# Optimization experiments

Hardware: AMD Instinct MI355X
Metric: run time of the kernel (lower is better)

## Reference

```python
import jax, jax.numpy as jnp
import numpy as np

ALPHA = 0.4  # LeakyReLU negative slope used by the GAT


def _gat_head(h, W, a):
    # h: [N, F], W: [F, Fp], a: [2*Fp]; adjacency is all-ones so no masking
    Wh = h @ W                                   # [N, Fp]
    Fp = W.shape[1]
    e = jax.nn.leaky_relu(Wh @ a[:Fp][:, None] + (Wh @ a[Fp:])[None, :], ALPHA)
    att = jax.nn.softmax(e, axis=-1)             # [N, N]
    return att @ Wh                              # [N, Fp]


def _gat(h, W_heads, a_heads, W_gout, a_gout):
    # multi-head GAT: concat elu(head outputs), then single output attention layer
    heads = jax.vmap(_gat_head, in_axes=(None, 0, 0))(h, W_heads, a_heads)  # [H, N, Fp]
    x = jax.nn.elu(heads).transpose(1, 0, 2).reshape(h.shape[0], -1)        # [N, H*Fp]
    return jax.nn.elu(_gat_head(x, W_gout, a_gout))                          # [N, Cg]


def setup_inputs() -> dict:
    key = jax.random.key(0)
    ks = jax.random.split(key, 20)
    bs, R, S = 4, 512, 54
    h, w = 100, 152
    fc_dim, convs_dim4 = 1024, 512
    Cg, H, So = 256, 4, 128
    Fp = Cg // H
    sc = lambda k, shp, s=0.05: jax.random.normal(k, shp, dtype=jnp.float32) * s
    return {
        'region_f': jax.random.normal(ks[0], (bs * R, fc_dim), dtype=jnp.float32),
        'stuff_f': jax.random.normal(ks[1], (bs, convs_dim4, h, w), dtype=jnp.float32),
        'semseg_score': jax.random.normal(ks[2], (bs, S, h, w), dtype=jnp.float32),
        'W_rin': sc(ks[3], (fc_dim, Cg)), 'b_rin': jnp.zeros((Cg,), jnp.float32),
        'W_sin': sc(ks[4], (convs_dim4, Cg)), 'b_sin': jnp.zeros((Cg,), jnp.float32),
        'W_heads': sc(ks[5], (H, Cg, Fp), 0.1), 'a_heads': sc(ks[6], (H, 2 * Fp), 0.1),
        'W_gout': sc(ks[7], (H * Fp, Cg), 0.1), 'a_gout': sc(ks[8], (2 * Cg,), 0.1),
        'W_rout': sc(ks[9], (Cg, Cg)), 'b_rout': jnp.zeros((Cg,), jnp.float32),
        'W_sout': sc(ks[10], (Cg, So)), 'b_sout': jnp.zeros((So,), jnp.float32),
        'W_seg': sc(ks[11], (convs_dim4 + So, S)), 'b_seg': jnp.zeros((S,), jnp.float32),
    }


def reference(region_f, stuff_f, semseg_score,
              W_rin, b_rin, W_sin, b_sin,
              W_heads, a_heads, W_gout, a_gout,
              W_rout, b_rout, W_sout, b_sout,
              W_seg, b_seg):
    bs, Cd, h, w = stuff_f.shape
    S = semseg_score.shape[1]
    R = region_f.shape[0] // bs
    Cg = W_rin.shape[1]

    # node construction
    region_nodes = region_f @ W_rin + b_rin                           # [bs*R, Cg]
    score_flat = semseg_score.reshape(bs, S, h * w)
    class_center = jnp.einsum('bsn,bcn->bsc',
                              jax.nn.softmax(score_flat, axis=-1),
                              stuff_f.reshape(bs, Cd, h * w))          # [bs, S, Cd]
    class_nodes = class_center @ W_sin + b_sin                         # [bs, S, Cg]

    # per-image dense GAT over region + stuff nodes (batched via vmap)
    nodes = jnp.concatenate([region_nodes.reshape(bs, R, Cg), class_nodes], axis=1)
    graph_nodes = jax.vmap(lambda x: _gat(x, W_heads, a_heads, W_gout, a_gout))(nodes)
    new_region, new_class = graph_nodes[:, :R], graph_nodes[:, R:]

    # new box features: concat of original region features and projected graph features
    new_region_f = jnp.concatenate(
        [region_f, new_region.reshape(bs * R, Cg) @ W_rout + b_rout], axis=-1)

    # new stuff features: scatter class nodes back to pixels via class softmax
    new_class_nodes = new_class @ W_sout + b_sout                      # [bs, S, So]
    attn = jax.nn.softmax(score_flat, axis=1)                          # softmax over classes
    new_stuff = jnp.einsum('bsn,bso->bon', attn, new_class_nodes)      # [bs, So, h*w]
    new_stuff = new_stuff.reshape(bs, -1, h, w)

    # 1x1 conv seg head + x4 bilinear upsample (align_corners=False)
    seg_in = jnp.concatenate([stuff_f, new_stuff], axis=1)
    seg = jnp.einsum('bchw,co->bohw', seg_in, W_seg) + b_seg[None, :, None, None]
    segments = jax.image.resize(seg, (bs, S, 4 * h, 4 * w), method='bilinear')
    return new_region_f, segments
```

## Files before the change

### kernel.cpp

```cpp
#include <hip/hip_runtime.h>

#define HW 15200
#define SSD 54
#define NBATCH 4
#define NNODE 566
#define NPAD 576
#define CGD 256
#define CDD 512
#define NSPLIT 25
#define KSPAN 608

typedef __attribute__((ext_vector_type(4))) float f32x4;
typedef __attribute__((ext_vector_type(8))) short bf16x8;
typedef unsigned short ushort_t;

#define BT_RIN   0
#define BT_SIN   262144
#define BT_HEADS 393216
#define BT_GOUT  458752
#define BT_ROUT  524288
#define BT_SOUT  589824
#define BT_SEG2  622592
#define BT_TOTAL 630784

static constexpr long OFF_P     = 0;
static constexpr long OFF_CC    = OFF_P     + (long)NBATCH*SSD*HW;
static constexpr long OFF_NODES = OFF_CC    + (long)NBATCH*SSD*CDD;
static constexpr long OFF_WH    = OFF_NODES + (long)NBATCH*NNODE*CGD;
static constexpr long OFF_S1    = OFF_WH    + (long)16*NNODE*64;
static constexpr long OFF_S2    = OFF_S1    + 16*NPAD;
static constexpr long OFF_X     = OFF_S2    + 16*NPAD;
static constexpr long OFF_WH2   = OFF_X     + (long)NBATCH*NNODE*CGD;
static constexpr long OFF_S1B   = OFF_WH2   + (long)NBATCH*NNODE*CGD;
static constexpr long OFF_S2B   = OFF_S1B   + NBATCH*NPAD;
static constexpr long OFF_G     = OFF_S2B   + NBATCH*NPAD;
static constexpr long OFF_NCN   = OFF_G     + (long)NBATCH*NNODE*CGD;
static constexpr long OFF_SUMS  = OFF_NCN   + (long)NBATCH*SSD*128;
static constexpr long OFF_BT    = OFF_SUMS  + 256;
static constexpr long OFF_ASEG  = OFF_BT    + (BT_TOTAL/2 + 8);
static constexpr long OFF_SEG   = OFF_ASEG  + (long)NBATCH*64*576/2;
static constexpr long OFF_RFB   = OFF_SEG   + (long)NBATCH*SSD*HW;
static constexpr long OFF_WCOMB = OFF_RFB   + 1048576;
static constexpr long OFF_B2    = OFF_WCOMB + 8192;
static constexpr long OFF_ATTNB = OFF_B2    + 64;

__device__ inline float lrelu04(float x){ return x >= 0.f ? x : 0.4f*x; }
__device__ inline float eluf(float x){ return x > 0.f ? x : __expf(x) - 1.f; }
__device__ inline ushort_t f2bf(float f){
    unsigned u = __float_as_uint(f);
    return (ushort_t)((u + 0x7FFFu + ((u >> 16) & 1u)) >> 16);
}
__device__ inline float bf2f(ushort_t u){ return __uint_as_float((unsigned)u << 16); }
__device__ inline bf16x8 pack8(float4 lo, float4 hi){
    union { bf16x8 v; ushort_t u[8]; } p;
    p.u[0]=f2bf(lo.x); p.u[1]=f2bf(lo.y); p.u[2]=f2bf(lo.z); p.u[3]=f2bf(lo.w);
    p.u[4]=f2bf(hi.x); p.u[5]=f2bf(hi.y); p.u[6]=f2bf(hi.z); p.u[7]=f2bf(hi.w);
    return p.v;
}

__global__ __launch_bounds__(512)
void prep_softmax(const float* __restrict__ score, ushort_t* __restrict__ pb,
                  float* __restrict__ sums, ushort_t* __restrict__ attnb,
                  const float* __restrict__ rf, float* __restrict__ out_region,
                  ushort_t* __restrict__ rfb,
                  const float* __restrict__ W_seg, ushort_t* __restrict__ asegb,
                  const float* __restrict__ W_rin, const float* __restrict__ W_sin,
                  const float* __restrict__ W_heads, const float* __restrict__ W_gout,
                  const float* __restrict__ W_rout, const float* __restrict__ W_sout,
                  const float* __restrict__ b_sout,
                  ushort_t* __restrict__ bt, ushort_t* __restrict__ wcomb,
                  float* __restrict__ bias2, float* __restrict__ s1s2b_zero)
{
    int blk = blockIdx.x;
    int t = threadIdx.x;
    if (blk < 256) {
        int b = blk >> 6, s = blk & 63;
        ushort_t* prow = pb + ((long)b*64 + s)*HW;
        if (s >= SSD) {
            for (int i = t; i < HW; i += 512) prow[i] = 0;
            if (t == 0) sums[b*64 + s] = 1.f;
            return;
        }
        const float* row = score + ((long)b*SSD + s)*HW;
        __shared__ float red[8];
        float s_ = 0.f;
        for (int i = t; i < HW; i += 512) {
            float e = __expf(row[i]);
            s_ += e;
            prow[i] = f2bf(e);
        }
        #pragma unroll
        for (int off = 32; off >= 1; off >>= 1) s_ += __shfl_down(s_, off);
        if ((t & 63) == 0) red[t >> 6] = s_;
        __syncthreads();
        if (t == 0) {
            float tot = 0.f;
            #pragma unroll
            for (int u = 0; u < 8; ++u) tot += red[u];
            sums[b*64 + s] = tot;
        }
        return;
    }
    if (blk < 375) {
        long i = (long)(blk - 256)*512 + t;
        if (i >= (long)NBATCH*HW) return;
        int b = (int)(i / HW), n = (int)(i % HW);
        const float* sp = score + (long)b*SSD*HW + n;
        float v[SSD];
        float m = -1e30f;
        #pragma unroll
        for (int s = 0; s < SSD; ++s) { v[s] = sp[(long)s*HW]; m = fmaxf(m, v[s]); }
        float sum = 0.f;
        #pragma unroll
        for (int s = 0; s < SSD; ++s) { v[s] = __expf(v[s] - m); sum += v[s]; }
        float inv = 1.f / sum;
        ushort_t* ap = attnb + (long)b*64*HW + n;
        #pragma unroll
        for (int s = 0; s < SSD; ++s) ap[(long)s*HW] = f2bf(v[s] * inv);
        #pragma unroll
        for (int s = SSD; s < 64; ++s) ap[(long)s*HW] = 0;
        return;
    }
    long gid = (long)(blk - 375) * 512 + t;
    if (gid < 524288) {
        long row = gid / 256, col = gid % 256;
        float4 v = reinterpret_cast<const float4*>(rf)[gid];
        reinterpret_cast<float4*>(out_region)[row*320 + col] = v;
        union { ushort_t u[4]; uint2 q; } pk;
        pk.u[0]=f2bf(v.x); pk.u[1]=f2bf(v.y); pk.u[2]=f2bf(v.z); pk.u[3]=f2bf(v.w);
        reinterpret_cast<uint2*>(rfb)[gid] = pk.q;
        return;
    }
    gid -= 524288;
    if (gid < 131072) {
        int b = (int)(gid >> 15);
        int r = (int)(gid & 32767);
        int o = r >> 9, k = r & 511;
        asegb[(long)b*36864 + (long)o*576 + k] = f2bf(o < SSD ? W_seg[k*SSD + o] : 0.f);
        return;
    }
    gid -= 131072;
    if (gid < BT_TOTAL) {
        int i = (int)gid;
        float v;
        if (i < BT_SIN)        { int j=i;            int n=j>>10, k=j&1023; v = W_rin[k*256+n]; }
        else if (i < BT_HEADS) { int j=i-BT_SIN;     int n=j>>9,  k=j&511;  v = W_sin[k*256+n]; }
        else if (i < BT_GOUT)  { int j=i-BT_HEADS;   int h=j>>14, r=j&16383; int f=r>>8, k=r&255;
                                 v = W_heads[(h*256+k)*64+f]; }
        else if (i < BT_ROUT)  { int j=i-BT_GOUT;    int n=j>>8,  k=j&255;  v = W_gout[k*256+n]; }
        else if (i < BT_SOUT)  { int j=i-BT_ROUT;    int n=j>>8,  k=j&255;  v = W_rout[k*256+n]; }
        else if (i < BT_SEG2)  { int j=i-BT_SOUT;    int n=j>>8,  k=j&255;  v = W_sout[k*128+n]; }
        else                   { int j=i-BT_SEG2;    int o=j>>7,  k=j&127;
                                 v = (o < SSD) ? W_seg[(512+k)*SSD + o] : 0.f; }
        bt[i] = f2bf(v);
        return;
    }
    gid -= BT_TOTAL;
    if (gid < 16384) {
        int od = (int)(gid >> 8), k = (int)(gid & 255);
        float v = 0.f;
        if (od < SSD)
            for (int o = 0; o < 128; ++o)
                v += W_sout[k*128 + o] * W_seg[(512+o)*SSD + od];
        wcomb[(long)od*256 + k] = f2bf(v);
        return;
    }
    gid -= 16384;
    if (gid < 64) {
        int od = (int)gid;
        float v = 0.f;
        if (od < SSD)
            for (int o = 0; o < 128; ++o)
                v += b_sout[o] * W_seg[(512+o)*SSD + od];
        bias2[od] = v;
        return;
    }
    gid -= 64;
    if (gid < 2L*NBATCH*NPAD)
        s1s2b_zero[gid] = 0.f;
}

__global__ __launch_bounds__(256)
void cc_mfma_v3(const ushort_t* __restrict__ pb, const float* __restrict__ stuff,
                ushort_t* __restrict__ sbout, float* __restrict__ part)
{
    int bid = blockIdx.x;
    int g = (bid >> 6) * 8 + (bid & 7);
    if (g >= NSPLIT*NBATCH) return;
    int nt = (bid >> 3) & 7;
    int ks = g >> 2, b = g & 3;

    int w = threadIdx.x >> 6, l = threadIdx.x & 63;
    int lr = l & 15, lk = l >> 4;
    int n0 = nt*64 + w*16;
    const ushort_t* Prow = pb + ((long)b*64 + lr)*HW;
    const float*    Srow = stuff + ((long)b*CDD + n0 + lr)*HW;
    ushort_t*       Sout = sbout + ((long)b*CDD + n0 + lr)*HW;
    f32x4 acc[4] = {};
    int kbeg = ks * KSPAN;
    for (int k0 = kbeg; k0 < kbeg + KSPAN; k0 += 32) {
        int kk = k0 + lk*8;
        float4 lo = *(const float4*)&Srow[kk];
        float4 hi = *(const float4*)&Srow[kk + 4];
        bf16x8 bfv = pack8(lo, hi);
        *(bf16x8*)&Sout[kk] = bfv;
        #pragma unroll
        for (int mi = 0; mi < 4; ++mi) {
            bf16x8 af = *(const bf16x8*)&Prow[(long)mi*16*HW + kk];
            acc[mi] = __builtin_amdgcn_mfma_f32_16x16x32_bf16(af, bfv, acc[mi], 0, 0, 0);
        }
    }
    int c = n0 + lr;
    #pragma unroll
    for (int mi = 0; mi < 4; ++mi)
        #pragma unroll
        for (int r = 0; r < 4; ++r) {
            int m = mi*16 + lk*4 + r;
            part[(((long)b*NSPLIT + ks)*64 + m)*CDD + c] = acc[mi][r];
        }
}

__global__ __launch_bounds__(256)
void cc_reduce_kernel(const float* __restrict__ part, const float* __restrict__ sums,
                      float* __restrict__ cc)
{
    long i = (long)blockIdx.x * 256 + threadIdx.x;
    const long TOT = (long)NBATCH * SSD * CDD;
    if (i >= TOT) return;
    int b = (int)(i / (SSD * CDD));
    int rem = (int)(i % (SSD * CDD));
    int s = rem / CDD, c = rem % CDD;
    float acc = 0.f;
    for (int ks = 0; ks < NSPLIT; ++ks)
        acc += part[(((long)b*NSPLIT + ks)*64 + s)*CDD + c];
    cc[i] = acc * (1.f / sums[b*64 + s]);
}

template<bool AF32, int OUTMODE>
__device__ __forceinline__
void mm_body(int bx, int by, int bz,
             const void* __restrict__ Ap, const ushort_t* __restrict__ Bt,
             void* __restrict__ Cp, const float* __restrict__ bias,
             int M, int N, int K, int lda, int ldc,
             long sA, int zdivA, long sB, int zmodB, long sC)
{
    int z = bz;
    int w = threadIdx.x >> 6, l = threadIdx.x & 63;
    int lr = l & 15, lk = l >> 4;
    int m0 = bx * 64 + w * 16;
    int n0 = by * 64;
    const ushort_t* bt = Bt + (long)(z % zmodB) * sB;
    int mload = min(m0 + lr, M - 1);
    const float*    Af = (const float*)Ap    + (long)(z / zdivA) * sA + (long)mload * lda;
    const ushort_t* Ab = (const ushort_t*)Ap + (long)(z / zdivA) * sA + (long)mload * lda;
    f32x4 acc[4] = {};

    #pragma unroll 2
    for (int k0 = 0; k0 < K; k0 += 32) {
        int kk = k0 + lk * 8;
        bf16x8 af;
        if (AF32) {
            float4 lo = *(const float4*)&Af[kk];
            float4 hi = *(const float4*)&Af[kk + 4];
            af = pack8(lo, hi);
        } else {
            af = *(const bf16x8*)&Ab[kk];
        }
        #pragma unroll
        for (int j = 0; j < 4; ++j) {
            bf16x8 bf = *(const bf16x8*)&bt[(long)(n0 + j*16 + lr) * K + kk];
            acc[j] = __builtin_amdgcn_mfma_f32_16x16x32_bf16(af, bf, acc[j], 0, 0, 0);
        }
    }

    #pragma unroll
    for (int j = 0; j < 4; ++j) {
        int n = n0 + j*16 + lr;
        float bb = bias ? bias[n] : 0.f;
        #pragma unroll
        for (int r = 0; r < 4; ++r) {
            int m = m0 + lk*4 + r;
            if (OUTMODE == 2) {
                float v = acc[j][r] + bb;
                ((ushort_t*)Cp)[(long)z * sC + (long)n * ldc + m] =
                    (m < M) ? f2bf(v) : (ushort_t)0;
            } else {
                if (m >= M) continue;
                float v = acc[j][r] + bb;
                if (OUTMODE == 0)
                    ((float*)Cp)[(long)z * sC + (long)m * ldc + n] = v;
                else
                    ((ushort_t*)Cp)[(long)z * sC + (long)m * ldc + n] = f2bf(v);
            }
        }
    }
}

template<bool AF32, int OUTMODE>
__global__ __launch_bounds__(256)
void mm_mfma(const void* __restrict__ Ap, const ushort_t* __restrict__ Bt,
             void* __restrict__ Cp, const float* __restrict__ bias,
             int M, int N, int K, int lda, int ldc,
             long sA, int zdivA, long sB, int zmodB, long sC)
{
    mm_body<AF32, OUTMODE>(blockIdx.x, blockIdx.y, blockIdx.z,
                           Ap, Bt, Cp, bias, M, N, K, lda, ldc,
                           sA, zdivA, sB, zmodB, sC);
}

__global__ __launch_bounds__(256)
void nodes_both(const ushort_t* __restrict__ rfb, const ushort_t* __restrict__ btRin,
                const float* __restrict__ cc, const ushort_t* __restrict__ btSin,
                ushort_t* __restrict__ nodes,
                const float* __restrict__ b_rin, const float* __restrict__ b_sin)
{
    if (blockIdx.x < 8)
        mm_body<false, 1>(blockIdx.x, blockIdx.y, blockIdx.z,
                          rfb, btRin, nodes, b_rin,
                          512, 256, 1024, 1024, 256, 512L*1024, 1, 0, 1, (long)NNODE*CGD);
    else
        mm_body<true, 1>(0, blockIdx.y, blockIdx.z,
                         cc, btSin, nodes + 512L*CGD, b_sin,
                         SSD, 256, 512, 512, 256, (long)SSD*CDD, 1, 0, 1, (long)NNODE*CGD);
}

__global__ __launch_bounds__(256)
void rout_m2(const ushort_t* __restrict__ g_bf, const ushort_t* __restrict__ btRout,
             float* __restrict__ outreg, const float* __restrict__ b_rout,
             const ushort_t* __restrict__ wcomb, ushort_t* __restrict__ asegm2,
             const float* __restrict__ bias2)
{
    if (blockIdx.x < 8)
        mm_body<false, 0>(blockIdx.x, blockIdx.y, blockIdx.z,
                          g_bf, btRout, outreg, b_rout,
                          512, 256, 256, 256, 1280, (long)NNODE*CGD, 1, 0, 1, 512L*1280);
    else if (blockIdx.y == 0)
        mm_body<false, 2>(0, 0, blockIdx.z,
                          g_bf + 512L*CGD, wcomb, asegm2, bias2,
                          SSD, 64, 256, 256, 576, (long)NNODE*CGD, 1, 0, 1, 36864L);
}

__global__ __launch_bounds__(256)
void wht_heads(const ushort_t* __restrict__ nodes, const ushort_t* __restrict__ btHeads,
               ushort_t* __restrict__ wht, const float* __restrict__ a_heads,
               float* __restrict__ s1, float* __restrict__ s2)
{
    int bx = blockIdx.x, z = blockIdx.y;
    int w = threadIdx.x >> 6, l = threadIdx.x & 63;
    int lr = l & 15, lk = l >> 4;
    int m0 = bx*64 + w*16;
    const ushort_t* bt = btHeads + (long)(z & 3) * (64L*256);
    int mload = min(m0 + lr, NNODE - 1);
    const ushort_t* Ab = nodes + (long)(z >> 2)*((long)NNODE*CGD) + (long)mload*CGD;
    f32x4 acc[4] = {};

    #pragma unroll 2
    for (int k0 = 0; k0 < 256; k0 += 32) {
        int kk = k0 + lk*8;
        bf16x8 af = *(const bf16x8*)&Ab[kk];
        #pragma unroll
        for (int j = 0; j < 4; ++j) {
            bf16x8 bf = *(const bf16x8*)&bt[(long)(j*16 + lr)*256 + kk];
            acc[j] = __builtin_amdgcn_mfma_f32_16x16x32_bf16(af, bf, acc[j], 0, 0, 0);
        }
    }

    const float* av = a_heads + (long)(z & 3)*128;
    ushort_t* Wout = wht + (long)z*(64L*NPAD);
    float p1[4] = {0.f,0.f,0.f,0.f}, p2[4] = {0.f,0.f,0.f,0.f};
    #pragma unroll
    for (int j = 0; j < 4; ++j) {
        int f = j*16 + lr;
        float c1 = av[f], c2 = av[64 + f];
        #pragma unroll
        for (int r = 0; r < 4; ++r) {
            int m = m0 + lk*4 + r;
            float v = acc[j][r];
            Wout[(long)f*NPAD + m] = (m < NNODE) ? f2bf(v) : (ushort_t)0;
            if (m < NNODE) { p1[r] += v*c1; p2[r] += v*c2; }
        }
    }
    #pragma unroll
    for (int r = 0; r < 4; ++r)
        #pragma unroll
        for (int off = 1; off < 16; off <<= 1) {
            p1[r] += __shfl_xor(p1[r], off);
            p2[r] += __shfl_xor(p2[r], off);
        }
    if (lr == 0) {
        #pragma unroll
        for (int r = 0; r < 4; ++r) {
            int m = m0 + lk*4 + r;
            if (m < NNODE) {
                s1[(long)z*NPAD + m] = p1[r];
                s2[(long)z*NPAD + m] = p2[r];
            }
        }
    }
}

__global__ __launch_bounds__(256)
void wht2_gout(const ushort_t* __restrict__ xbuf, const ushort_t* __restrict__ btGout,
               ushort_t* __restrict__ wht2, const float* __restrict__ a_gout,
               float* __restrict__ s1b, float* __restrict__ s2b)
{
    int bx = blockIdx.x, by = blockIdx.y, z = blockIdx.z;
    int w = threadIdx.x >> 6, l = threadIdx.x & 63;
    int lr = l & 15, lk = l >> 4;
    int m0 = bx*64 + w*16;
    int n0 = by*64;
    int mload = min(m0 + lr, NNODE - 1);
    const ushort_t* Ab = xbuf + (long)z*((long)NNODE*CGD) + (long)mload*CGD;
    f32x4 acc[4] = {};

    #pragma unroll 2
    for (int k0 = 0; k0 < 256; k0 += 32) {
        int kk = k0 + lk*8;
        bf16x8 af = *(const bf16x8*)&Ab[kk];
        #pragma unroll
        for (int j = 0; j < 4; ++j) {
            bf16x8 bf = *(const bf16x8*)&btGout[(long)(n0 + j*16 + lr)*256 + kk];
            acc[j] = __builtin_amdgcn_mfma_f32_16x16x32_bf16(af, bf, acc[j], 0, 0, 0);
        }
    }

    ushort_t* Wout = wht2 + (long)z*(256L*NPAD);
    float p1[4] = {0.f,0.f,0.f,0.f}, p2[4] = {0.f,0.f,0.f,0.f};
    #pragma unroll
    for (int j = 0; j < 4; ++j) {
        int f = n0 + j*16 + lr;
        float c1 = a_gout[f], c2 = a_gout[256 + f];
        #pragma unroll
        for (int r = 0; r < 4; ++r) {
            int m = m0 + lk*4 + r;
            float v = acc[j][r];
            Wout[(long)f*NPAD + m] = (m < NNODE) ? f2bf(v) : (ushort_t)0;
            if (m < NNODE) { p1[r] += v*c1; p2[r] += v*c2; }
        }
    }
    #pragma unroll
    for (int r = 0; r < 4; ++r)
        #pragma unroll
        for (int off = 1; off < 16; off <<= 1) {
            p1[r] += __shfl_xor(p1[r], off);
            p2[r] += __shfl_xor(p2[r], off);
        }
    if (lr == 0) {
        #pragma unroll
        for (int r = 0; r < 4; ++r) {
            int m = m0 + lk*4 + r;
            if (m < NNODE) {
                atomicAdd(&s1b[(long)z*NPAD + m], p1[r]);
                atomicAdd(&s2b[(long)z*NPAD + m], p2[r]);
            }
        }
    }
}

template<int F, int HEADMODE>
__global__ __launch_bounds__(256)
void att_mfma(const ushort_t* __restrict__ WhTall, const float* __restrict__ s1v,
              const float* __restrict__ s2v, ushort_t* __restrict__ outbuf)
{
    constexpr int FT = F / 16;
    int z = blockIdx.y;
    const ushort_t* W  = WhTall + (long)z * F * NPAD;
    const float* s1 = s1v + (long)z * NPAD;
    const float* s2 = s2v + (long)z * NPAD;
    int w = threadIdx.x >> 6, l = threadIdx.x & 63;
    int lr = l & 15, lk = l >> 4;

    __shared__ float s2sh[NPAD];
    __shared__ float redm[4];
    float mxl = -1e30f;
    for (int i = threadIdx.x; i < NPAD; i += 256) {
        float v = (i < NNODE) ? s2[i] : -1e30f;
        s2sh[i] = v;
        mxl = fmaxf(mxl, v);
    }
    #pragma unroll
    for (int off = 32; off >= 1; off >>= 1) mxl = fmaxf(mxl, __shfl_down(mxl, off));
    if (l == 0) redm[w] = mxl;
    __syncthreads();
    float s2max = fmaxf(fmaxf(redm[0], redm[1]), fmaxf(redm[2], redm[3]));

    int m0 = blockIdx.x * 64 + w * 16;
    float s1r = s1[min(m0 + lr, NNODE - 1)];
    float mrow = lrelu04(s1r + s2max);

    union { bf16x8 v; ushort_t u[8]; } onesu;
    #pragma unroll
    for (int u = 0; u < 8; ++u) onesu.u[u] = 0x3F80;
    bf16x8 ones = onesu.v;

    f32x4 acc[FT] = {};
    f32x4 accw = {};

    for (int j0 = 0; j0 < NPAD; j0 += 32) {
        float wv[8];
        #pragma unroll
        for (int u = 0; u < 8; ++u) {
            float e = lrelu04(s1r + s2sh[j0 + lk*8 + u]);
            wv[u] = __expf(e - mrow);
        }
        float4 lo = {wv[0], wv[1], wv[2], wv[3]};
        float4 hi = {wv[4], wv[5], wv[6], wv[7]};
        bf16x8 af = pack8(lo, hi);
        accw = __builtin_amdgcn_mfma_f32_16x16x32_bf16(af, ones, accw, 0, 0, 0);
        #pragma unroll
        for (int ft = 0; ft < FT; ++ft) {
            bf16x8 bf = *(const bf16x8*)&W[(long)(ft*16 + lr)*NPAD + j0 + lk*8];
            acc[ft] = __builtin_amdgcn_mfma_f32_16x16x32_bf16(af, bf, acc[ft], 0, 0, 0);
        }
    }

    #pragma unroll
    for (int r = 0; r < 4; ++r) {
        int m = m0 + lk*4 + r;
        if (m >= NNODE) continue;
        float inv = 1.f / accw[r];
        #pragma unroll
        for (int ft = 0; ft < FT; ++ft) {
            int f = ft*16 + lr;
            float v = eluf(acc[ft][r] * inv);
            if (HEADMODE) {
                int b = z >> 2, h = z & 3;
                outbuf[((long)(b*NNODE + m))*CGD + h*64 + f] = f2bf(v);
            } else {
                outbuf[((long)(z*NNODE + m))*CGD + f] = f2bf(v);
            }
        }
    }
}

__global__ __launch_bounds__(256)
void seg_mfma(const ushort_t* __restrict__ stuffb, const ushort_t* __restrict__ attnb,
              const ushort_t* __restrict__ asegb, const float* __restrict__ b_seg,
              float* __restrict__ seg)
{
    int nt = blockIdx.x, b = blockIdx.y;
    int w = threadIdx.x >> 6, l = threadIdx.x & 63;
    int lr = l & 15, lk = l >> 4;
    int n0 = nt*128 + w*32;
    const ushort_t* A = asegb + (long)b*36864;
    const ushort_t* S = stuffb + (long)b*CDD*HW;
    const ushort_t* T = attnb + (long)b*64*HW;
    f32x4 acc[4][2] = {};
    int n1 = min(n0 + lr, HW-1);
    int n2 = min(n0 + 16 + lr, HW-1);

    for (int k0 = 0; k0 < 576; k0 += 32) {
        const ushort_t* Bsrc = (k0 < 512) ? S + (long)k0*HW : T + (long)(k0-512)*HW;
        long kb = (long)(lk*8)*HW;
        union { bf16x8 v; ushort_t u[8]; } b0, b1;
        #pragma unroll
        for (int u = 0; u < 8; ++u) {
            b0.u[u] = Bsrc[kb + (long)u*HW + n1];
            b1.u[u] = Bsrc[kb + (long)u*HW + n2];
        }
        #pragma unroll
        for (int ot = 0; ot < 4; ++ot) {
            bf16x8 af = *(const bf16x8*)&A[(ot*16 + lr)*576 + k0 + lk*8];
            acc[ot][0] = __builtin_amdgcn_mfma_f32_16x16x32_bf16(af, b0.v, acc[ot][0], 0,0,0);
            acc[ot][1] = __builtin_amdgcn_mfma_f32_16x16x32_bf16(af, b1.v, acc[ot][1], 0,0,0);
        }
    }

    #pragma unroll
    for (int ot = 0; ot < 4; ++ot) {
        #pragma unroll
        for (int r = 0; r < 4; ++r) {
            int o = ot*16 + lk*4 + r;
            if (o >= SSD) continue;
            float bb = b_seg[o];
            int na = n0 + lr, nb = n0 + 16 + lr;
            if (na < HW) seg[((long)b*SSD + o)*HW + na] = acc[ot][0][r] + bb;
            if (nb < HW) seg[((long)b*SSD + o)*HW + nb] = acc[ot][1][r] + bb;
        }
    }
}

__global__ __launch_bounds__(256)
void resize_v2_kernel(const float* __restrict__ seg, float* __restrict__ out)
{
    long u = (long)blockIdx.x * 256 + threadIdx.x;
    const long TOT4 = (long)NBATCH * SSD * 400 * 152;
    if (u >= TOT4) return;
    int m = (int)(u % 152);
    long r = u / 152;
    int y = (int)(r % 400);
    long c = r / 400;
    float fy = y * 0.25f - 0.375f;
    int y0 = (int)floorf(fy);
    float wy = fy - (float)y0;
    int y0c = max(y0, 0), y1c = min(y0 + 1, 99);
    const float* sp = seg + c * HW;
    int xm = max(m - 1, 0), xp = min(m + 1, 151);
    float r0a = sp[y0c * 152 + xm], r0b = sp[y0c * 152 + m], r0c = sp[y0c * 152 + xp];
    float r1a = sp[y1c * 152 + xm], r1b = sp[y1c * 152 + m], r1c = sp[y1c * 152 + xp];
    float ra = r0a + wy * (r1a - r0a);
    float rb = r0b + wy * (r1b - r0b);
    float rc = r0c + wy * (r1c - r0c);
    float4 o4;
    o4.x = 0.375f * ra + 0.625f * rb;
    o4.y = 0.125f * ra + 0.875f * rb;
    o4.z = 0.875f * rb + 0.125f * rc;
    o4.w = 0.625f * rb + 0.375f * rc;
    reinterpret_cast<float4*>(out)[u] = o4;
}

extern "C" void kernel_launch(void* const* d_in, const int* in_sizes, int n_in,
                              void* d_out, int out_size, void* d_ws, size_t ws_size,
                              hipStream_t stream)
{
    const float* region_f = (const float*)d_in[0];
    const float* stuff    = (const float*)d_in[1];
    const float* score    = (const float*)d_in[2];
    const float* W_rin    = (const float*)d_in[3];
    const float* b_rin    = (const float*)d_in[4];
    const float* W_sin    = (const float*)d_in[5];
    const float* b_sin    = (const float*)d_in[6];
    const float* W_heads  = (const float*)d_in[7];
    const float* a_heads  = (const float*)d_in[8];
    const float* W_gout   = (const float*)d_in[9];
    const float* a_gout   = (const float*)d_in[10];
    const float* W_rout   = (const float*)d_in[11];
    const float* b_rout   = (const float*)d_in[12];
    const float* W_sout   = (const float*)d_in[13];
    const float* b_sout   = (const float*)d_in[14];
    const float* W_seg    = (const float*)d_in[15];
    const float* b_seg    = (const float*)d_in[16];

    float* out = (float*)d_out;
    float* ws  = (float*)d_ws;

    ushort_t* pb   = (ushort_t*)(ws + OFF_P);
    float* cc      = ws + OFF_CC;
    ushort_t* nodes_bf = (ushort_t*)(ws + OFF_NODES);
    ushort_t* wht  = (ushort_t*)(ws + OFF_WH);
    float* s1      = ws + OFF_S1;
    float* s2      = ws + OFF_S2;
    ushort_t* xbuf_bf = (ushort_t*)(ws + OFF_X);
    ushort_t* wht2 = (ushort_t*)(ws + OFF_WH2);
    float* s1b     = ws + OFF_S1B;
    float* s2b     = ws + OFF_S2B;
    ushort_t* g_bf = (ushort_t*)(ws + OFF_G);
    float* sums    = ws + OFF_SUMS;
    ushort_t* bt   = (ushort_t*)(ws + OFF_BT);
    ushort_t* asegb = (ushort_t*)(ws + OFF_ASEG);
    float* segb    = ws + OFF_SEG;
    float* cc_p    = ws + OFF_SEG;
    ushort_t* rfb  = (ushort_t*)(ws + OFF_RFB);
    ushort_t* wcomb = (ushort_t*)(ws + OFF_WCOMB);
    float* bias2v  = ws + OFF_B2;
    ushort_t* attnb = (ushort_t*)(ws + OFF_ATTNB);

    float* out_region = out;
    float* out_seg    = out + 2048L*1280;
    ushort_t* stuffb  = (ushort_t*)out_seg;

    prep_softmax<<<2929, 512, 0, stream>>>(score, pb, sums, attnb,
                                           region_f, out_region, rfb, W_seg, asegb,
                                           W_rin, W_sin, W_heads, W_gout, W_rout, W_sout,
                                           b_sout, bt, wcomb, bias2v, s1b);

    cc_mfma_v3<<<832, 256, 0, stream>>>(pb, stuff, stuffb, cc_p);
    cc_reduce_kernel<<<(NBATCH*SSD*CDD + 255)/256, 256, 0, stream>>>(cc_p, sums, cc);

    nodes_both<<<dim3(9, 4, 4), 256, 0, stream>>>(
        rfb, bt + BT_RIN, cc, bt + BT_SIN, nodes_bf, b_rin, b_sin);

    wht_heads<<<dim3(9, 16), 256, 0, stream>>>(
        nodes_bf, bt + BT_HEADS, wht, a_heads, s1, s2);

    att_mfma<64, 1><<<dim3(9, 16), 256, 0, stream>>>(wht, s1, s2, xbuf_bf);

    wht2_gout<<<dim3(9, 4, 4), 256, 0, stream>>>(
        xbuf_bf, bt + BT_GOUT, wht2, a_gout, s1b, s2b);

    att_mfma<256, 0><<<dim3(9, NBATCH), 256, 0, stream>>>(wht2, s1b, s2b, g_bf);

    rout_m2<<<dim3(9, 4, 4), 256, 0, stream>>>(
        g_bf, bt + BT_ROUT, out_region + 1024, b_rout, wcomb, asegb + 512, bias2v);

    seg_mfma<<<dim3((HW+127)/128, NBATCH), 256, 0, stream>>>(
        stuffb, attnb, asegb, b_seg, segb);

    resize_v2_kernel<<<((long)NBATCH*SSD*400*152 + 255)/256, 256, 0, stream>>>(segb, out_seg);
}
```

Before: 321.9 us.

## Fuse GAT attention, gout projection, and rout/seg stages into fewer kernels

Merges the per-head attention with the output-layer weight projection into one kernel per batch, keeping head outputs in shared memory instead of a global buffer. Folds the class-node seg-weight projection into the output attention kernel, and merges the region output GEMM with the seg head GEMM into one launch. Replaces atomics with direct stores, which removes the zeroing pass. This cuts launches and global round-trips, but the fused graph kernels run on far fewer blocks with more serial work per block.

```diff
diff --git a/kernel.cpp b/kernel.cpp
--- a/kernel.cpp
+++ b/kernel.cpp
@@ -69,7 +69,7 @@
                   const float* __restrict__ W_rout, const float* __restrict__ W_sout,
                   const float* __restrict__ b_sout,
                   ushort_t* __restrict__ bt, ushort_t* __restrict__ wcomb,
-                  float* __restrict__ bias2, float* __restrict__ s1s2b_zero)
+                  float* __restrict__ bias2)
 {
     int blk = blockIdx.x;
     int t = threadIdx.x;
@@ -173,11 +173,7 @@
             for (int o = 0; o < 128; ++o)
                 v += b_sout[o] * W_seg[(512+o)*SSD + od];
         bias2[od] = v;
-        return;
-    }
-    gid -= 64;
-    if (gid < 2L*NBATCH*NPAD)
-        s1s2b_zero[gid] = 0.f;
+    }
 }
 
 __global__ __launch_bounds__(256)
@@ -296,18 +292,6 @@
     }
 }
 
-template<bool AF32, int OUTMODE>
-__global__ __launch_bounds__(256)
-void mm_mfma(const void* __restrict__ Ap, const ushort_t* __restrict__ Bt,
-             void* __restrict__ Cp, const float* __restrict__ bias,
-             int M, int N, int K, int lda, int ldc,
-             long sA, int zdivA, long sB, int zmodB, long sC)
-{
-    mm_body<AF32, OUTMODE>(blockIdx.x, blockIdx.y, blockIdx.z,
-                           Ap, Bt, Cp, bias, M, N, K, lda, ldc,
-                           sA, zdivA, sB, zmodB, sC);
-}
-
 __global__ __launch_bounds__(256)
 void nodes_both(const ushort_t* __restrict__ rfb, const ushort_t* __restrict__ btRin,
                 const float* __restrict__ cc, const ushort_t* __restrict__ btSin,
@@ -325,22 +309,6 @@
 }
 
 __global__ __launch_bounds__(256)
-void rout_m2(const ushort_t* __restrict__ g_bf, const ushort_t* __restrict__ btRout,
-             float* __restrict__ outreg, const float* __restrict__ b_rout,
-             const ushort_t* __restrict__ wcomb, ushort_t* __restrict__ asegm2,
-             const float* __restrict__ bias2)
-{
-    if (blockIdx.x < 8)
-        mm_body<false, 0>(blockIdx.x, blockIdx.y, blockIdx.z,
-                          g_bf, btRout, outreg, b_rout,
-                          512, 256, 256, 256, 1280, (long)NNODE*CGD, 1, 0, 1, 512L*1280);
-    else if (blockIdx.y == 0)
-        mm_body<false, 2>(0, 0, blockIdx.z,
-                          g_bf + 512L*CGD, wcomb, asegm2, bias2,
-                          SSD, 64, 256, 256, 576, (long)NNODE*CGD, 1, 0, 1, 36864L);
-}
-
-__global__ __launch_bounds__(256)
 void wht_heads(const ushort_t* __restrict__ nodes, const ushort_t* __restrict__ btHeads,
                ushort_t* __restrict__ wht, const float* __restrict__ a_heads,
                float* __restrict__ s1, float* __restrict__ s2)
@@ -400,42 +368,105 @@
 }
 
 __global__ __launch_bounds__(256)
-void wht2_gout(const ushort_t* __restrict__ xbuf, const ushort_t* __restrict__ btGout,
-               ushort_t* __restrict__ wht2, const float* __restrict__ a_gout,
-               float* __restrict__ s1b, float* __restrict__ s2b)
-{
-    int bx = blockIdx.x, by = blockIdx.y, z = blockIdx.z;
-    int w = threadIdx.x >> 6, l = threadIdx.x & 63;
+void att64_wht2(const ushort_t* __restrict__ whtAll, const float* __restrict__ s1v,
+                const float* __restrict__ s2v, const ushort_t* __restrict__ btGout,
+                ushort_t* __restrict__ wht2, const float* __restrict__ a_gout,
+                float* __restrict__ s1b, float* __restrict__ s2b)
+{
+    int bx = blockIdx.x, b = blockIdx.y;
+    int t = threadIdx.x;
+    int w = t >> 6, l = t & 63;
     int lr = l & 15, lk = l >> 4;
     int m0 = bx*64 + w*16;
-    int n0 = by*64;
-    int mload = min(m0 + lr, NNODE - 1);
-    const ushort_t* Ab = xbuf + (long)z*((long)NNODE*CGD) + (long)mload*CGD;
-    f32x4 acc[4] = {};
-
-    #pragma unroll 2
-    for (int k0 = 0; k0 < 256; k0 += 32) {
-        int kk = k0 + lk*8;
-        bf16x8 af = *(const bf16x8*)&Ab[kk];
-        #pragma unroll
-        for (int j = 0; j < 4; ++j) {
-            bf16x8 bf = *(const bf16x8*)&btGout[(long)(n0 + j*16 + lr)*256 + kk];
-            acc[j] = __builtin_amdgcn_mfma_f32_16x16x32_bf16(af, bf, acc[j], 0, 0, 0);
-        }
-    }
-
-    ushort_t* Wout = wht2 + (long)z*(256L*NPAD);
-    float p1[4] = {0.f,0.f,0.f,0.f}, p2[4] = {0.f,0.f,0.f,0.f};
-    #pragma unroll
-    for (int j = 0; j < 4; ++j) {
-        int f = n0 + j*16 + lr;
-        float c1 = a_gout[f], c2 = a_gout[256 + f];
+
+    __shared__ float s2sh[4][NPAD];
+    __shared__ float s2maxsh[4];
+    __shared__ ushort_t xst[64][264];
+
+    for (int i = t; i < 4*NPAD; i += 256) {
+        int h = i / NPAD, j = i % NPAD;
+        s2sh[h][j] = (j < NNODE) ? s2v[((long)(b*4 + h))*NPAD + j] : -1e30f;
+    }
+    if (bx == 8)
+        for (int i = t; i < 10*264; i += 256) xst[54 + i/264][i%264] = 0;
+    __syncthreads();
+    {
+        float mx = -1e30f;
+        for (int q = 0; q < 9; ++q) mx = fmaxf(mx, s2sh[w][l + 64*q]);
+        #pragma unroll
+        for (int off = 32; off >= 1; off >>= 1) mx = fmaxf(mx, __shfl_down(mx, off));
+        if (l == 0) s2maxsh[w] = mx;
+    }
+    __syncthreads();
+
+    union { bf16x8 v; ushort_t u[8]; } onesu;
+    #pragma unroll
+    for (int u = 0; u < 8; ++u) onesu.u[u] = 0x3F80;
+    bf16x8 ones = onesu.v;
+
+    for (int h = 0; h < 4; ++h) {
+        const ushort_t* W = whtAll + (long)(b*4 + h)*(64L*NPAD);
+        float s1r = s1v[(long)(b*4 + h)*NPAD + min(m0 + lr, NNODE - 1)];
+        float mrow = lrelu04(s1r + s2maxsh[h]);
+        f32x4 acc[4] = {};
+        f32x4 accw = {};
+        for (int j0 = 0; j0 < NPAD; j0 += 32) {
+            float wv[8];
+            #pragma unroll
+            for (int u = 0; u < 8; ++u) {
+                float e = lrelu04(s1r + s2sh[h][j0 + lk*8 + u]);
+                wv[u] = __expf(e - mrow);
+            }
+            float4 lo = {wv[0], wv[1], wv[2], wv[3]};
+            float4 hi = {wv[4], wv[5], wv[6], wv[7]};
+            bf16x8 af = pack8(lo, hi);
+            accw = __builtin_amdgcn_mfma_f32_16x16x32_bf16(af, ones, accw, 0, 0, 0);
+            #pragma unroll
+            for (int ft = 0; ft < 4; ++ft) {
+                bf16x8 bf = *(const bf16x8*)&W[(long)(ft*16 + lr)*NPAD + j0 + lk*8];
+                acc[ft] = __builtin_amdgcn_mfma_f32_16x16x32_bf16(af, bf, acc[ft], 0, 0, 0);
+            }
+        }
         #pragma unroll
         for (int r = 0; r < 4; ++r) {
             int m = m0 + lk*4 + r;
-            float v = acc[j][r];
-            Wout[(long)f*NPAD + m] = (m < NNODE) ? f2bf(v) : (ushort_t)0;
-            if (m < NNODE) { p1[r] += v*c1; p2[r] += v*c2; }
+            if (m >= NNODE) continue;
+            float inv = 1.f / accw[r];
+            #pragma unroll
+            for (int ft = 0; ft < 4; ++ft) {
+                int f = ft*16 + lr;
+                xst[w*16 + lk*4 + r][h*64 + f] = f2bf(eluf(acc[ft][r] * inv));
+            }
+        }
+    }
+    __syncthreads();
+
+    float p1[4] = {0.f,0.f,0.f,0.f}, p2[4] = {0.f,0.f,0.f,0.f};
+    ushort_t* Wout = wht2 + (long)b*(256L*NPAD);
+    for (int y = 0; y < 4; ++y) {
+        int n0 = y*64;
+        f32x4 acc2[4] = {};
+        #pragma unroll 2
+        for (int k0 = 0; k0 < 256; k0 += 32) {
+            int kk = k0 + lk*8;
+            bf16x8 af = *(const bf16x8*)&xst[w*16 + lr][kk];
+            #pragma unroll
+            for (int j = 0; j < 4; ++j) {
+                bf16x8 bf = *(const bf16x8*)&btGout[(long)(n0 + j*16 + lr)*256 + kk];
+                acc2[j] = __builtin_amdgcn_mfma_f32_16x16x32_bf16(af, bf, acc2[j], 0, 0, 0);
+            }
+        }
+        #pragma unroll
+        for (int j = 0; j < 4; ++j) {
+            int f = n0 + j*16 + lr;
+            float c1 = a_gout[f], c2 = a_gout[256 + f];
+            #pragma unroll
+            for (int r = 0; r < 4; ++r) {
+                int m = m0 + lk*4 + r;
+                float v = acc2[j][r];
+                Wout[(long)f*NPAD + m] = (m < NNODE) ? f2bf(v) : (ushort_t)0;
+                if (m < NNODE) { p1[r] += v*c1; p2[r] += v*c2; }
+            }
         }
     }
     #pragma unroll
@@ -450,41 +481,46 @@
         for (int r = 0; r < 4; ++r) {
             int m = m0 + lk*4 + r;
             if (m < NNODE) {
-                atomicAdd(&s1b[(long)z*NPAD + m], p1[r]);
-                atomicAdd(&s2b[(long)z*NPAD + m], p2[r]);
-            }
-        }
-    }
-}
-
-template<int F, int HEADMODE>
+                s1b[(long)b*NPAD + m] = p1[r];
+                s2b[(long)b*NPAD + m] = p2[r];
+            }
+        }
+    }
+}
+
 __global__ __launch_bounds__(256)
-void att_mfma(const ushort_t* __restrict__ WhTall, const float* __restrict__ s1v,
-              const float* __restrict__ s2v, ushort_t* __restrict__ outbuf)
-{
-    constexpr int FT = F / 16;
-    int z = blockIdx.y;
-    const ushort_t* W  = WhTall + (long)z * F * NPAD;
+void att_gout_m2(const ushort_t* __restrict__ wht2, const float* __restrict__ s1v,
+                 const float* __restrict__ s2v, ushort_t* __restrict__ g,
+                 const ushort_t* __restrict__ wcomb, const float* __restrict__ bias2,
+                 ushort_t* __restrict__ asegm2)
+{
+    int bx = blockIdx.x, z = blockIdx.y;
+    const ushort_t* W  = wht2 + (long)z * (256L*NPAD);
     const float* s1 = s1v + (long)z * NPAD;
     const float* s2 = s2v + (long)z * NPAD;
-    int w = threadIdx.x >> 6, l = threadIdx.x & 63;
+    int t = threadIdx.x;
+    int w = t >> 6, l = t & 63;
     int lr = l & 15, lk = l >> 4;
 
     __shared__ float s2sh[NPAD];
     __shared__ float redm[4];
+    __shared__ ushort_t gld[64][264];
+
     float mxl = -1e30f;
-    for (int i = threadIdx.x; i < NPAD; i += 256) {
+    for (int i = t; i < NPAD; i += 256) {
         float v = (i < NNODE) ? s2[i] : -1e30f;
         s2sh[i] = v;
         mxl = fmaxf(mxl, v);
     }
+    if (bx == 8)
+        for (int i = t; i < 10*264; i += 256) gld[54 + i/264][i%264] = 0;
     #pragma unroll
     for (int off = 32; off >= 1; off >>= 1) mxl = fmaxf(mxl, __shfl_down(mxl, off));
     if (l == 0) redm[w] = mxl;
     __syncthreads();
     float s2max = fmaxf(fmaxf(redm[0], redm[1]), fmaxf(redm[2], redm[3]));
 
-    int m0 = blockIdx.x * 64 + w * 16;
+    int m0 = bx * 64 + w * 16;
     float s1r = s1[min(m0 + lr, NNODE - 1)];
     float mrow = lrelu04(s1r + s2max);
 
@@ -493,7 +529,7 @@
     for (int u = 0; u < 8; ++u) onesu.u[u] = 0x3F80;
     bf16x8 ones = onesu.v;
 
-    f32x4 acc[FT] = {};
+    f32x4 acc[16] = {};
     f32x4 accw = {};
 
     for (int j0 = 0; j0 < NPAD; j0 += 32) {
@@ -508,7 +544,7 @@
         bf16x8 af = pack8(lo, hi);
         accw = __builtin_amdgcn_mfma_f32_16x16x32_bf16(af, ones, accw, 0, 0, 0);
         #pragma unroll
-        for (int ft = 0; ft < FT; ++ft) {
+        for (int ft = 0; ft < 16; ++ft) {
             bf16x8 bf = *(const bf16x8*)&W[(long)(ft*16 + lr)*NPAD + j0 + lk*8];
             acc[ft] = __builtin_amdgcn_mfma_f32_16x16x32_bf16(af, bf, acc[ft], 0, 0, 0);
         }
@@ -520,25 +556,47 @@
         if (m >= NNODE) continue;
         float inv = 1.f / accw[r];
         #pragma unroll
-        for (int ft = 0; ft < FT; ++ft) {
+        for (int ft = 0; ft < 16; ++ft) {
             int f = ft*16 + lr;
-            float v = eluf(acc[ft][r] * inv);
-            if (HEADMODE) {
-                int b = z >> 2, h = z & 3;
-                outbuf[((long)(b*NNODE + m))*CGD + h*64 + f] = f2bf(v);
-            } else {
-                outbuf[((long)(z*NNODE + m))*CGD + f] = f2bf(v);
-            }
-        }
-    }
-}
-
-__global__ __launch_bounds__(256)
-void seg_mfma(const ushort_t* __restrict__ stuffb, const ushort_t* __restrict__ attnb,
+            ushort_t vb = f2bf(eluf(acc[ft][r] * inv));
+            g[((long)(z*NNODE + m))*CGD + f] = vb;
+            if (bx == 8) gld[m - 512][f] = vb;
+        }
+    }
+
+    if (bx == 8) {
+        __syncthreads();
+        f32x4 acc2[4] = {};
+        #pragma unroll 2
+        for (int k0 = 0; k0 < 256; k0 += 32) {
+            int kk = k0 + lk*8;
+            bf16x8 af = *(const bf16x8*)&gld[w*16 + lr][kk];
+            #pragma unroll
+            for (int j = 0; j < 4; ++j) {
+                bf16x8 bf = *(const bf16x8*)&wcomb[(long)(j*16 + lr)*256 + kk];
+                acc2[j] = __builtin_amdgcn_mfma_f32_16x16x32_bf16(af, bf, acc2[j], 0, 0, 0);
+            }
+        }
+        #pragma unroll
+        for (int j = 0; j < 4; ++j) {
+            int n = j*16 + lr;
+            float bb = bias2[n];
+            #pragma unroll
+            for (int r = 0; r < 4; ++r) {
+                int m = w*16 + lk*4 + r;
+                asegm2[(long)z*36864 + (long)n*576 + m] =
+                    (m < SSD) ? f2bf(acc2[j][r] + bb) : (ushort_t)0;
+            }
+        }
+    }
+}
+
+__device__ __forceinline__
+void seg_body(int nt, int b,
+              const ushort_t* __restrict__ stuffb, const ushort_t* __restrict__ attnb,
               const ushort_t* __restrict__ asegb, const float* __restrict__ b_seg,
               float* __restrict__ seg)
 {
-    int nt = blockIdx.x, b = blockIdx.y;
     int w = threadIdx.x >> 6, l = threadIdx.x & 63;
     int lr = l & 15, lk = l >> 4;
     int n0 = nt*128 + w*32;
@@ -577,6 +635,24 @@
             if (na < HW) seg[((long)b*SSD + o)*HW + na] = acc[ot][0][r] + bb;
             if (nb < HW) seg[((long)b*SSD + o)*HW + nb] = acc[ot][1][r] + bb;
         }
+    }
+}
+
+__global__ __launch_bounds__(256)
+void rout_seg(const ushort_t* __restrict__ g_bf, const ushort_t* __restrict__ btRout,
+              float* __restrict__ outreg, const float* __restrict__ b_rout,
+              const ushort_t* __restrict__ stuffb, const ushort_t* __restrict__ attnb,
+              const ushort_t* __restrict__ asegb, const float* __restrict__ b_seg,
+              float* __restrict__ segb)
+{
+    int bid = blockIdx.x;
+    if (bid < 128) {
+        int x = bid & 7, y = (bid >> 3) & 3, z = bid >> 5;
+        mm_body<false, 0>(x, y, z, g_bf, btRout, outreg, b_rout,
+                          512, 256, 256, 256, 1280, (long)NNODE*CGD, 1, 0, 1, 512L*1280);
+    } else {
+        int sid = bid - 128;
+        seg_body(sid % 119, sid / 119, stuffb, attnb, asegb, b_seg, segb);
     }
 }
 
@@ -640,7 +716,6 @@
     ushort_t* wht  = (ushort_t*)(ws + OFF_WH);
     float* s1      = ws + OFF_S1;
     float* s2      = ws + OFF_S2;
-    ushort_t* xbuf_bf = (ushort_t*)(ws + OFF_X);
     ushort_t* wht2 = (ushort_t*)(ws + OFF_WH2);
     float* s1b     = ws + OFF_S1B;
     float* s2b     = ws + OFF_S2B;
@@ -659,10 +734,10 @@
     float* out_seg    = out + 2048L*1280;
     ushort_t* stuffb  = (ushort_t*)out_seg;
 
-    prep_softmax<<<2929, 512, 0, stream>>>(score, pb, sums, attnb,
+    prep_softmax<<<2920, 512, 0, stream>>>(score, pb, sums, attnb,
                                            region_f, out_region, rfb, W_seg, asegb,
                                            W_rin, W_sin, W_heads, W_gout, W_rout, W_sout,
-                                           b_sout, bt, wcomb, bias2v, s1b);
+                                           b_sout, bt, wcomb, bias2v);
 
     cc_mfma_v3<<<832, 256, 0, stream>>>(pb, stuff, stuffb, cc_p);
     cc_reduce_kernel<<<(NBATCH*SSD*CDD + 255)/256, 256, 0, stream>>>(cc_p, sums, cc);
@@ -673,17 +748,14 @@
     wht_heads<<<dim3(9, 16), 256, 0, stream>>>(
         nodes_bf, bt + BT_HEADS, wht, a_heads, s1, s2);
 
-    att_mfma<64, 1><<<dim3(9, 16), 256, 0, stream>>>(wht, s1, s2, xbuf_bf);
-
-    wht2_gout<<<dim3(9, 4, 4), 256, 0, stream>>>(
-        xbuf_bf, bt + BT_GOUT, wht2, a_gout, s1b, s2b);
-
-    att_mfma<256, 0><<<dim3(9, NBATCH), 256, 0, stream>>>(wht2, s1b, s2b, g_bf);
-
-    rout_m2<<<dim3(9, 4, 4), 256, 0, stream>>>(
-        g_bf, bt + BT_ROUT, out_region + 1024, b_rout, wcomb, asegb + 512, bias2v);
-
-    seg_mfma<<<dim3((HW+127)/128, NBATCH), 256, 0, stream>>>(
+    att64_wht2<<<dim3(9, 4), 256, 0, stream>>>(
+        wht, s1, s2, bt + BT_GOUT, wht2, a_gout, s1b, s2b);
+
+    att_gout_m2<<<dim3(9, 4), 256, 0, stream>>>(
+        wht2, s1b, s2b, g_bf, wcomb, bias2v, asegb + 512);
+
+    rout_seg<<<604, 256, 0, stream>>>(
+        g_bf, bt + BT_ROUT, out_region + 1024, b_rout,
         stuffb, attnb, asegb, b_seg, segb);
 
     resize_v2_kernel<<<((long)NBATCH*SSD*400*152 + 255)/256, 256, 0, stream>>>(segb, out_seg);
```

Result: slower. 358.4 us (+11.3%).
